# Performance work log

Measured on AMD Instinct MI355X. Metric: run time of the kernel, lower is better.

The kernel has to match this reference:

```python
import jax, jax.numpy as jnp
import numpy as np
import math

D = 1024
B, S = 4, 2048


def setup_inputs() -> dict:
    key = jax.random.key(0)
    ks = jax.random.split(key, 16)
    sc = 0.02
    def lin(k, dout, din):
        kw, kb = jax.random.split(k)
        return (sc * jax.random.normal(kw, (dout, din), jnp.float32),
                sc * jax.random.normal(kb, (dout,), jnp.float32))
    Wq, bq = lin(ks[0], D, D)
    Wk, bk = lin(ks[1], D, D)
    Wv, bv = lin(ks[2], D, D)
    Wmu, bmu = lin(ks[3], D, D)
    Wlv, blv = lin(ks[4], D, D)
    Wg, bg = lin(ks[5], 1, D)
    gamma = jnp.ones((D,), jnp.float32)
    beta = jnp.zeros((D,), jnp.float32)
    x = jax.random.normal(ks[6], (B, S, D), jnp.float32)
    eps = jax.random.normal(ks[7], (B, S, D), jnp.float32)
    return dict(x=x, eps=eps, Wq=Wq, bq=bq, Wk=Wk, bk=bk, Wv=Wv, bv=bv,
                Wmu=Wmu, bmu=bmu, Wlv=Wlv, blv=blv, Wg=Wg, bg=bg,
                gamma=gamma, beta=beta)


def _layernorm(x, gamma, beta, eps=1e-5):
    mu = jnp.mean(x, axis=-1, keepdims=True)
    var = jnp.mean(jnp.square(x - mu), axis=-1, keepdims=True)
    return (x - mu) * jax.lax.rsqrt(var + eps) * gamma + beta


def reference(x, eps, Wq, bq, Wk, bk, Wv, bv, Wmu, bmu, Wlv, blv, Wg, bg, gamma, beta):
    d = x.shape[-1]
    Q = jnp.einsum('bsd,ed->bse', x, Wq) + bq
    K = jnp.einsum('bsd,ed->bse', x, Wk) + bk
    V = jnp.einsum('bsd,ed->bse', x, Wv) + bv
    scores = jnp.einsum('bqd,bkd->bqk', Q, K) / (math.sqrt(d) * 1.5)
    attn = jax.nn.softmax(scores, axis=-1)
    h = jnp.einsum('bqk,bkd->bqd', attn, V)
    mu = jnp.einsum('bsd,ed->bse', h, Wmu) + bmu
    logvar = jnp.einsum('bsd,ed->bse', h, Wlv) + blv
    std = jnp.exp(0.5 * logvar)
    z = jax.nn.relu(mu + eps * std)
    p_gate = jax.nn.sigmoid(jnp.einsum('bd,ed->be', h.mean(axis=1), Wg) + bg)
    out = _layernorm(x + z, gamma, beta)
    return out, mu, logvar, p_gate.squeeze(-1)
```

## Files before the change

### kernel.cpp

```cpp
#include <hip/hip_runtime.h>

typedef unsigned short u16;
typedef __attribute__((ext_vector_type(8))) short bf16x8;
typedef __attribute__((ext_vector_type(4))) float f32x4;

__device__ inline float bf2f(u16 h) {
    union { unsigned u; float f; } v; v.u = ((unsigned)h) << 16; return v.f;
}
__device__ inline u16 f2bf(float f) {
    union { float f; unsigned u; } v; v.f = f;
    unsigned r = v.u + 0x7fffu + ((v.u >> 16) & 1u);
    return (u16)(r >> 16);
}

__device__ inline void gl_lds16(const u16* g, u16* l) {
    __builtin_amdgcn_global_load_lds(
        (const __attribute__((address_space(1))) void*)g,
        (__attribute__((address_space(3))) void*)l, 16, 0, 0);
}

__global__ __launch_bounds__(256) void cvt_bf16_k(
    const float* __restrict__ s0, u16* __restrict__ d0, long long n0,
    const float* __restrict__ s1, u16* __restrict__ d1, long long n1,
    const float* __restrict__ s2, u16* __restrict__ d2, long long n2,
    const float* __restrict__ s3, u16* __restrict__ d3, long long n3)
{
    int y = blockIdx.y;
    const float* s = (y == 0) ? s0 : (y == 1) ? s1 : (y == 2) ? s2 : s3;
    u16* d         = (y == 0) ? d0 : (y == 1) ? d1 : (y == 2) ? d2 : d3;
    long long n    = (y == 0) ? n0 : (y == 1) ? n1 : (y == 2) ? n2 : n3;
    for (long long i = (long long)blockIdx.x * 256 + threadIdx.x; i < n;
         i += (long long)gridDim.x * 256) {
        float4 v = ((const float4*)s)[i];
        union { u16 h[4]; unsigned long long u; } p;
        p.h[0] = f2bf(v.x); p.h[1] = f2bf(v.y);
        p.h[2] = f2bf(v.z); p.h[3] = f2bf(v.w);
        ((unsigned long long*)d)[i] = p.u;
    }
}

#define BM 128
#define BN 128
#define BK 32

template <int COUTF32, int BIASROW>
__global__ __launch_bounds__(256, 2) void gemm_bt(
    const u16* __restrict__ A, const u16* __restrict__ Bt,
    const float* __restrict__ bias, void* __restrict__ Cv,
    int M, int N, int K, float scale,
    long long sAb, long long sBb, long long sCb)
{
    __shared__ u16 As[BM * BK];
    __shared__ u16 Bs[BN * BK];

    int b = blockIdx.z;
    int bm0 = blockIdx.x * BM;
    int bn0 = blockIdx.y * BN;
    int tid = threadIdx.x;
    int w = tid >> 6, l = tid & 63;
    int wm = (w >> 1) * 64, wn = (w & 1) * 64;
    int lane15 = l & 15, quad = l >> 4;
    int lr = l >> 2;
    int lc = (l & 3) * 8;

    f32x4 acc[4][4];
#pragma unroll
    for (int i = 0; i < 4; i++)
#pragma unroll
        for (int j = 0; j < 4; j++) acc[i][j] = (f32x4)(0.0f);

    const u16* Ag = A  + (long long)b * sAb + (long long)(bm0 + w * 32 + lr) * K + lc;
    const u16* Bg = Bt + (long long)b * sBb + (long long)(bn0 + w * 32 + lr) * K + lc;

    for (int k0 = 0; k0 < K; k0 += BK) {
        gl_lds16(Ag + k0,            &As[(w * 32) * BK]);
        gl_lds16(Ag + 16LL * K + k0, &As[(w * 32 + 16) * BK]);
        gl_lds16(Bg + k0,            &Bs[(w * 32) * BK]);
        gl_lds16(Bg + 16LL * K + k0, &Bs[(w * 32 + 16) * BK]);
        __syncthreads();

        bf16x8 af[4], bfr[4];
#pragma unroll
        for (int i = 0; i < 4; i++) {
            af[i]  = *(const bf16x8*)&As[(wm + i * 16 + lane15) * BK + quad * 8];
            bfr[i] = *(const bf16x8*)&Bs[(wn + i * 16 + lane15) * BK + quad * 8];
        }
#pragma unroll
        for (int i = 0; i < 4; i++)
#pragma unroll
            for (int j = 0; j < 4; j++)
                acc[i][j] = __builtin_amdgcn_mfma_f32_16x16x32_bf16(
                    af[i], bfr[j], acc[i][j], 0, 0, 0);
        __syncthreads();
    }

    float rowb[4][4];
    if (BIASROW) {
#pragma unroll
        for (int i = 0; i < 4; i++)
#pragma unroll
            for (int r = 0; r < 4; r++)
                rowb[i][r] = bias[bm0 + wm + i * 16 + quad * 4 + r];
    }
    u16*   C16 = (u16*)Cv   + (long long)b * sCb;
    float* C32 = (float*)Cv + (long long)b * sCb;
#pragma unroll
    for (int j = 0; j < 4; j++) {
        int col = bn0 + wn + j * 16 + lane15;
        float bvc = (!BIASROW && bias) ? bias[col] : 0.0f;
#pragma unroll
        for (int i = 0; i < 4; i++) {
            int row0 = bm0 + wm + i * 16 + quad * 4;
#pragma unroll
            for (int r = 0; r < 4; r++) {
                float bv = BIASROW ? rowb[i][r] : bvc;
                float v = acc[i][j][r] * scale + bv;
                if (COUTF32) C32[(long long)(row0 + r) * N + col] = v;
                else         C16[(long long)(row0 + r) * N + col] = f2bf(v);
            }
        }
    }
}

__global__ __launch_bounds__(256) void softmax_k(u16* __restrict__ Sc)
{
    long long row = blockIdx.x;
    u16* s = Sc + row * 2048;
    int t = threadIdx.x;

    uint4 raw = *(const uint4*)(s + t * 8);
    const u16* rp = (const u16*)&raw;
    float v[8];
    float mx = -3.4e38f;
#pragma unroll
    for (int j = 0; j < 8; j++) { v[j] = bf2f(rp[j]); mx = fmaxf(mx, v[j]); }
#pragma unroll
    for (int o = 32; o > 0; o >>= 1) mx = fmaxf(mx, __shfl_xor(mx, o));
    __shared__ float redm[4];
    if ((t & 63) == 0) redm[t >> 6] = mx;
    __syncthreads();
    mx = fmaxf(fmaxf(redm[0], redm[1]), fmaxf(redm[2], redm[3]));

    float sum = 0.0f;
#pragma unroll
    for (int j = 0; j < 8; j++) { v[j] = __expf(v[j] - mx); sum += v[j]; }
#pragma unroll
    for (int o = 32; o > 0; o >>= 1) sum += __shfl_xor(sum, o);
    __shared__ float reds[4];
    if ((t & 63) == 0) reds[t >> 6] = sum;
    __syncthreads();
    sum = reds[0] + reds[1] + reds[2] + reds[3];

    float inv = 1.0f / sum;
    u16 o8[8];
#pragma unroll
    for (int j = 0; j < 8; j++) o8[j] = f2bf(v[j] * inv);
    *(uint4*)(s + t * 8) = *(const uint4*)o8;
}

__global__ __launch_bounds__(256) void gate_partial(const u16* __restrict__ h,
                                                    const float* __restrict__ Wg,
                                                    float* __restrict__ part)
{
    int b = blockIdx.x, c = blockIdx.y;
    int t = threadIdx.x;
    int tx = t & 127;
    int ty = t >> 7;
    int d0 = tx * 8;
    const u16* hb = h + (long long)b * 2048 * 1024 + (long long)c * 16 * 1024;

    float wg[8];
#pragma unroll
    for (int j = 0; j < 8; j++) wg[j] = Wg[d0 + j];

    float acc = 0.0f;
    for (int s = ty; s < 16; s += 2) {
        bf16x8 hv = *(const bf16x8*)&hb[(long long)s * 1024 + d0];
        const u16* hp = (const u16*)&hv;
#pragma unroll
        for (int j = 0; j < 8; j++) acc += bf2f(hp[j]) * wg[j];
    }
#pragma unroll
    for (int o = 32; o > 0; o >>= 1) acc += __shfl_xor(acc, o);
    __shared__ float red[4];
    if ((t & 63) == 0) red[t >> 6] = acc;
    __syncthreads();
    if (t == 0) part[b * 128 + c] = red[0] + red[1] + red[2] + red[3];
}

__global__ void gate_final(const float* __restrict__ part,
                           const float* __restrict__ bg, float* __restrict__ outp)
{
    int t = threadIdx.x;
    if (t < 4) {
        float s = 0.0f;
        for (int c = 0; c < 128; c++) s += part[t * 128 + c];
        float v = s * (1.0f / 2048.0f) + bg[0];
        outp[t] = 1.0f / (1.0f + __expf(-v));
    }
}

__global__ __launch_bounds__(256) void epilogue_k(
    const float* __restrict__ x, const float* __restrict__ ep,
    const float* __restrict__ mu, const float* __restrict__ lv,
    const float* __restrict__ gamma, const float* __restrict__ beta,
    float* __restrict__ out)
{
    long long base = (long long)blockIdx.x * 1024;
    int t = threadIdx.x;
    float y[4];
    float sum = 0.0f, sq = 0.0f;
#pragma unroll
    for (int j = 0; j < 4; j++) {
        int i = j * 256 + t;
        float xv = x[base + i];
        float ev = ep[base + i];
        float m  = mu[base + i];
        float sd = __expf(0.5f * lv[base + i]);
        float z  = fmaxf(m + ev * sd, 0.0f);
        float yy = xv + z;
        y[j] = yy; sum += yy; sq += yy * yy;
    }
#pragma unroll
    for (int o = 32; o > 0; o >>= 1) { sum += __shfl_xor(sum, o); sq += __shfl_xor(sq, o); }
    __shared__ float rs[4], rq[4];
    if ((t & 63) == 0) { rs[t >> 6] = sum; rq[t >> 6] = sq; }
    __syncthreads();
    sum = rs[0] + rs[1] + rs[2] + rs[3];
    sq  = rq[0] + rq[1] + rq[2] + rq[3];
    float mean = sum * (1.0f / 1024.0f);
    float var  = fmaxf(sq * (1.0f / 1024.0f) - mean * mean, 0.0f);
    float rstd = rsqrtf(var + 1e-5f);
#pragma unroll
    for (int j = 0; j < 4; j++) {
        int i = j * 256 + t;
        out[base + i] = (y[j] - mean) * rstd * gamma[i] + beta[i];
    }
}

extern "C" void kernel_launch(void* const* d_in, const int* in_sizes, int n_in,
                              void* d_out, int out_size, void* d_ws, size_t ws_size,
                              hipStream_t stream)
{
    const float* x     = (const float*)d_in[0];
    const float* ep    = (const float*)d_in[1];
    const float* Wq    = (const float*)d_in[2];
    const float* bq    = (const float*)d_in[3];
    const float* Wk    = (const float*)d_in[4];
    const float* bk    = (const float*)d_in[5];
    const float* Wv    = (const float*)d_in[6];
    const float* bv    = (const float*)d_in[7];
    const float* Wmu   = (const float*)d_in[8];
    const float* bmu   = (const float*)d_in[9];
    const float* Wlv   = (const float*)d_in[10];
    const float* blv   = (const float*)d_in[11];
    const float* Wg    = (const float*)d_in[12];
    const float* bg    = (const float*)d_in[13];
    const float* gamma = (const float*)d_in[14];
    const float* beta  = (const float*)d_in[15];
    float* out = (float*)d_out;

    const int M = 8192;
    const int D = 1024;
    const int S = 2048;

    float* mu_out = out + 8388608LL;
    float* lv_out = out + 16777216LL;
    float* pg_out = out + 25165824LL;

    u16* xb   = (u16*)out;
    u16* Wqb  = (u16*)out + 8388608LL;
    u16* Wkb  = (u16*)out + 9437184LL;
    u16* Wvb  = (u16*)out + 10485760LL;
    u16* Sc   = (u16*)out;
    u16* Q    = (u16*)mu_out;
    u16* Kb   = (u16*)mu_out + 8388608LL;
    u16* Vt   = (u16*)lv_out + 8388608LL;
    u16* h    = (u16*)d_ws;
    float* part = (float*)out;
    u16* Wmub = (u16*)out + 2097152LL;
    u16* Wlvb = (u16*)out + 3145728LL;

    dim3 blk(256);

    cvt_bf16_k<<<dim3(2048, 4), blk, 0, stream>>>(
        x,  xb,  2097152LL,
        Wq, Wqb, 262144LL,
        Wk, Wkb, 262144LL,
        Wv, Wvb, 262144LL);

    gemm_bt<0, 0><<<dim3(64, 8, 1), blk, 0, stream>>>(xb, Wqb, bq, Q,  M, D, D, 1.0f, 0, 0, 0);
    gemm_bt<0, 0><<<dim3(64, 8, 1), blk, 0, stream>>>(xb, Wkb, bk, Kb, M, D, D, 1.0f, 0, 0, 0);

    gemm_bt<0, 1><<<dim3(8, 16, 4), blk, 0, stream>>>(Wvb, xb, bv, Vt, D, S, D,
        1.0f, 0, (long long)S * D, (long long)D * S);

    gemm_bt<0, 0><<<dim3(16, 16, 4), blk, 0, stream>>>(Q, Kb, nullptr, Sc, S, S, D,
        1.0f / 48.0f, (long long)S * D, (long long)S * D, (long long)S * S);

    softmax_k<<<dim3(8192), blk, 0, stream>>>(Sc);

    gemm_bt<0, 0><<<dim3(16, 8, 4), blk, 0, stream>>>(Sc, Vt, nullptr, h, S, D, S,
        1.0f, (long long)S * S, (long long)D * S, (long long)S * D);

    cvt_bf16_k<<<dim3(512, 2), blk, 0, stream>>>(
        Wmu, Wmub, 262144LL,
        Wlv, Wlvb, 262144LL,
        nullptr, nullptr, 0LL,
        nullptr, nullptr, 0LL);

    gemm_bt<1, 0><<<dim3(64, 8, 1), blk, 0, stream>>>(h, Wmub, bmu, (void*)mu_out, M, D, D, 1.0f, 0, 0, 0);
    gemm_bt<1, 0><<<dim3(64, 8, 1), blk, 0, stream>>>(h, Wlvb, blv, (void*)lv_out, M, D, D, 1.0f, 0, 0, 0);

    gate_partial<<<dim3(4, 128), blk, 0, stream>>>(h, Wg, part);
    gate_final<<<dim3(1), dim3(64), 0, stream>>>(part, bg, pg_out);

    epilogue_k<<<dim3(8192), blk, 0, stream>>>(x, ep, mu_out, lv_out, gamma, beta, out);
}
```

Measured before the change: 457.7 us.

## Replace GEMM with 256x256 double-buffered 8-wave pipelined kernel and fuse projections

```diff
diff --git a/kernel.cpp b/kernel.cpp
--- a/kernel.cpp
+++ b/kernel.cpp
@@ -18,6 +18,13 @@
         (const __attribute__((address_space(1))) void*)g,
         (__attribute__((address_space(3))) void*)l, 16, 0, 0);
 }
+
+__device__ __forceinline__ void wgbar() {
+    asm volatile("" ::: "memory");
+    __builtin_amdgcn_s_barrier();
+    asm volatile("" ::: "memory");
+}
+#define VMW(n) asm volatile("s_waitcnt vmcnt(" #n ")" ::: "memory")
 
 __global__ __launch_bounds__(256) void cvt_bf16_k(
     const float* __restrict__ s0, u16* __restrict__ d0, long long n0,
@@ -39,84 +46,143 @@
     }
 }
 
-#define BM 128
-#define BN 128
-#define BK 32
-
-template <int COUTF32, int BIASROW>
-__global__ __launch_bounds__(256, 2) void gemm_bt(
+#define STA(T, H)                                                             \
+    { const u16* g_ = Ag + (long long)((H) * 128 + w * 8 + srow) * K          \
+                      + (T) * 64 + scol;                                      \
+      u16* l_ = (u16*)&As[(T) & 1][H][w * 512];                               \
+      gl_lds16(g_, l_);                                                       \
+      gl_lds16(g_ + (long long)64 * K, l_ + 4096); }
+
+#define STB(T, H)                                                             \
+    { const u16* g_ = Bg + (long long)(bn0 + (H) * 128 + w * 8 + srow) * ldb  \
+                      + (T) * 64 + scol;                                      \
+      u16* l_ = (u16*)&Bs[(T) & 1][H][w * 512];                               \
+      gl_lds16(g_, l_);                                                       \
+      gl_lds16(g_ + (long long)64 * ldb, l_ + 4096); }
+
+#define G8_PHASE(T, MQ, NQ, STAGES, WAITS)                                    \
+    {                                                                         \
+        bf16x8 av[4][2], bvv[2][2];                                           \
+        _Pragma("unroll")                                                     \
+        for (int ii = 0; ii < 4; ii++) {                                      \
+            int row = (MQ) * 64 + ii * 16 + lane15;                           \
+            _Pragma("unroll")                                                 \
+            for (int ks = 0; ks < 2; ks++)                                    \
+                av[ii][ks] = *(const bf16x8*)&As[(T) & 1][wm2]                \
+                    [(row * 64 + ks * 32 + quad * 8) ^ xr];                   \
+        }                                                                     \
+        _Pragma("unroll")                                                     \
+        for (int jj = 0; jj < 2; jj++) {                                      \
+            int row = (wn2 & 1) * 64 + (NQ) * 32 + jj * 16 + lane15;          \
+            _Pragma("unroll")                                                 \
+            for (int ks = 0; ks < 2; ks++)                                    \
+                bvv[jj][ks] = *(const bf16x8*)&Bs[(T) & 1][wn2 >> 1]          \
+                    [(row * 64 + ks * 32 + quad * 8) ^ xr];                   \
+        }                                                                     \
+        STAGES;                                                               \
+        WAITS;                                                                \
+        wgbar();                                                              \
+        __builtin_amdgcn_s_setprio(1);                                        \
+        _Pragma("unroll")                                                     \
+        for (int ii = 0; ii < 4; ii++)                                        \
+            _Pragma("unroll")                                                 \
+            for (int jj = 0; jj < 2; jj++) {                                  \
+                acc[(MQ)*4+ii][(NQ)*2+jj] =                                   \
+                    __builtin_amdgcn_mfma_f32_16x16x32_bf16(                  \
+                        av[ii][0], bvv[jj][0], acc[(MQ)*4+ii][(NQ)*2+jj],     \
+                        0, 0, 0);                                             \
+                acc[(MQ)*4+ii][(NQ)*2+jj] =                                   \
+                    __builtin_amdgcn_mfma_f32_16x16x32_bf16(                  \
+                        av[ii][1], bvv[jj][1], acc[(MQ)*4+ii][(NQ)*2+jj],     \
+                        0, 0, 0);                                             \
+            }                                                                 \
+        __builtin_amdgcn_s_setprio(0);                                        \
+        wgbar();                                                              \
+    }
+
+template <int COUTF32, int BIASROW, int NSPLIT>
+__global__ __launch_bounds__(512, 2) void gemm8(
     const u16* __restrict__ A, const u16* __restrict__ Bt,
-    const float* __restrict__ bias, void* __restrict__ Cv,
-    int M, int N, int K, float scale,
-    long long sAb, long long sBb, long long sCb)
-{
-    __shared__ u16 As[BM * BK];
-    __shared__ u16 Bs[BN * BK];
-
-    int b = blockIdx.z;
-    int bm0 = blockIdx.x * BM;
-    int bn0 = blockIdx.y * BN;
+    const float* __restrict__ bias0, const float* __restrict__ bias1,
+    const float* __restrict__ bias2,
+    void* __restrict__ C0, void* __restrict__ C1, void* __restrict__ C2,
+    int M, int N, int K, int ldb, float scale,
+    long long sAb, long long sBb, long long sCb, long long bofs_stride)
+{
+    __shared__ u16 As[2][2][8192];
+    __shared__ u16 Bs[2][2][8192];
+
+    int b   = blockIdx.z;
+    int bm0 = blockIdx.x * 256;
+    int bn0 = blockIdx.y * 256;
     int tid = threadIdx.x;
     int w = tid >> 6, l = tid & 63;
-    int wm = (w >> 1) * 64, wn = (w & 1) * 64;
+    int wm2 = w >> 2;
+    int wn2 = w & 3;
     int lane15 = l & 15, quad = l >> 4;
-    int lr = l >> 2;
-    int lc = (l & 3) * 8;
-
-    f32x4 acc[4][4];
-#pragma unroll
-    for (int i = 0; i < 4; i++)
+    int xr = (l & 7) << 3;
+
+    int srow = l >> 3;
+    int scol = ((l & 7) ^ (srow & 7)) * 8;
+
+    const u16* Ag = A  + (long long)b * sAb + (long long)bm0 * K;
+    const u16* Bg = Bt + (long long)b * sBb + (long long)(bm0 >> 11) * bofs_stride;
+
+    f32x4 acc[8][4];
+#pragma unroll
+    for (int i = 0; i < 8; i++)
 #pragma unroll
         for (int j = 0; j < 4; j++) acc[i][j] = (f32x4)(0.0f);
 
-    const u16* Ag = A  + (long long)b * sAb + (long long)(bm0 + w * 32 + lr) * K + lc;
-    const u16* Bg = Bt + (long long)b * sBb + (long long)(bn0 + w * 32 + lr) * K + lc;
-
-    for (int k0 = 0; k0 < K; k0 += BK) {
-        gl_lds16(Ag + k0,            &As[(w * 32) * BK]);
-        gl_lds16(Ag + 16LL * K + k0, &As[(w * 32 + 16) * BK]);
-        gl_lds16(Bg + k0,            &Bs[(w * 32) * BK]);
-        gl_lds16(Bg + 16LL * K + k0, &Bs[(w * 32 + 16) * BK]);
-        __syncthreads();
-
-        bf16x8 af[4], bfr[4];
-#pragma unroll
-        for (int i = 0; i < 4; i++) {
-            af[i]  = *(const bf16x8*)&As[(wm + i * 16 + lane15) * BK + quad * 8];
-            bfr[i] = *(const bf16x8*)&Bs[(wn + i * 16 + lane15) * BK + quad * 8];
-        }
-#pragma unroll
-        for (int i = 0; i < 4; i++)
-#pragma unroll
-            for (int j = 0; j < 4; j++)
-                acc[i][j] = __builtin_amdgcn_mfma_f32_16x16x32_bf16(
-                    af[i], bfr[j], acc[i][j], 0, 0, 0);
-        __syncthreads();
-    }
-
-    float rowb[4][4];
+    int NT  = K >> 6;
+    int NT2 = K >> 7;
+
+    STA(0, 0); STA(0, 1); STB(0, 0); STB(0, 1); STA(1, 1);
+    VMW(2);
+    wgbar();
+
+    for (int j = 0; j < NT2; ++j) {
+        int t0 = 2 * j, t1 = 2 * j + 1;
+        bool nl = (j < NT2 - 1);
+        G8_PHASE(t0, 0, 0, STA(t1, 0), );
+        G8_PHASE(t0, 0, 1, STB(t1, 0), );
+        G8_PHASE(t0, 1, 1, STB(t1, 1), );
+        G8_PHASE(t0, 1, 0, if (nl) STA(t0 + 2, 0),
+                 if (nl) { VMW(2); } else { VMW(0); });
+        G8_PHASE(t1, 1, 0, if (nl) STA(t0 + 2, 1), );
+        G8_PHASE(t1, 1, 1, if (nl) STB(t0 + 2, 0), );
+        G8_PHASE(t1, 0, 1, if (nl) STB(t0 + 2, 1), );
+        G8_PHASE(t1, 0, 0, if (nl) STA(t0 + 3, 1),
+                 if (nl) { VMW(2); } else { VMW(0); });
+    }
+
+    float rowb_[8][4];
     if (BIASROW) {
 #pragma unroll
-        for (int i = 0; i < 4; i++)
+        for (int i = 0; i < 8; i++)
 #pragma unroll
             for (int r = 0; r < 4; r++)
-                rowb[i][r] = bias[bm0 + wm + i * 16 + quad * 4 + r];
-    }
-    u16*   C16 = (u16*)Cv   + (long long)b * sCb;
-    float* C32 = (float*)Cv + (long long)b * sCb;
-#pragma unroll
-    for (int j = 0; j < 4; j++) {
-        int col = bn0 + wn + j * 16 + lane15;
-        float bvc = (!BIASROW && bias) ? bias[col] : 0.0f;
-#pragma unroll
-        for (int i = 0; i < 4; i++) {
-            int row0 = bm0 + wm + i * 16 + quad * 4;
+                rowb_[i][r] = bias0[bm0 + wm2 * 128 + i * 16 + quad * 4 + r];
+    }
+#pragma unroll
+    for (int jj = 0; jj < 4; jj++) {
+        int col = bn0 + wn2 * 64 + jj * 16 + lane15;
+        int seg, cl, cstride;
+        if (NSPLIT == 1) { seg = 0; cl = col; cstride = N; }
+        else             { seg = col >> 10; cl = col & 1023; cstride = 1024; }
+        const float* bp = (seg == 0) ? bias0 : (seg == 1 ? bias1 : bias2);
+        void* cb = (seg == 0) ? C0 : (seg == 1 ? C1 : C2);
+        u16*   c16 = (u16*)cb   + (long long)b * sCb;
+        float* c32 = (float*)cb + (long long)b * sCb;
+        float bvc = (!BIASROW && bp) ? bp[cl] : 0.0f;
+#pragma unroll
+        for (int i = 0; i < 8; i++) {
+            int row0 = bm0 + wm2 * 128 + i * 16 + quad * 4;
 #pragma unroll
             for (int r = 0; r < 4; r++) {
-                float bv = BIASROW ? rowb[i][r] : bvc;
-                float v = acc[i][j][r] * scale + bv;
-                if (COUTF32) C32[(long long)(row0 + r) * N + col] = v;
-                else         C16[(long long)(row0 + r) * N + col] = f2bf(v);
+                float v = acc[i][jj][r] * scale + (BIASROW ? rowb_[i][r] : bvc);
+                if (COUTF32) c32[(long long)(row0 + r) * cstride + cl] = v;
+                else         c16[(long long)(row0 + r) * cstride + cl] = f2bf(v);
             }
         }
     }
@@ -275,13 +341,13 @@
     u16* Sc   = (u16*)out;
     u16* Q    = (u16*)mu_out;
     u16* Kb   = (u16*)mu_out + 8388608LL;
-    u16* Vt   = (u16*)lv_out + 8388608LL;
+    u16* Vt   = (u16*)lv_out;
     u16* h    = (u16*)d_ws;
     float* part = (float*)out;
     u16* Wmub = (u16*)out + 2097152LL;
     u16* Wlvb = (u16*)out + 3145728LL;
 
-    dim3 blk(256);
+    dim3 blk(256), blk8(512);
 
     cvt_bf16_k<<<dim3(2048, 4), blk, 0, stream>>>(
         x,  xb,  2097152LL,
@@ -289,19 +355,24 @@
         Wk, Wkb, 262144LL,
         Wv, Wvb, 262144LL);
 
-    gemm_bt<0, 0><<<dim3(64, 8, 1), blk, 0, stream>>>(xb, Wqb, bq, Q,  M, D, D, 1.0f, 0, 0, 0);
-    gemm_bt<0, 0><<<dim3(64, 8, 1), blk, 0, stream>>>(xb, Wkb, bk, Kb, M, D, D, 1.0f, 0, 0, 0);
-
-    gemm_bt<0, 1><<<dim3(8, 16, 4), blk, 0, stream>>>(Wvb, xb, bv, Vt, D, S, D,
-        1.0f, 0, (long long)S * D, (long long)D * S);
-
-    gemm_bt<0, 0><<<dim3(16, 16, 4), blk, 0, stream>>>(Q, Kb, nullptr, Sc, S, S, D,
-        1.0f / 48.0f, (long long)S * D, (long long)S * D, (long long)S * S);
+    gemm8<0, 0, 2><<<dim3(32, 8, 1), blk8, 0, stream>>>(
+        xb, Wqb, bq, bk, nullptr, Q, Kb, nullptr,
+        M, 2048, D, D, 1.0f, 0, 0, 0, 0);
+
+    gemm8<0, 1, 1><<<dim3(4, 32, 1), blk8, 0, stream>>>(
+        Wvb, xb, bv, nullptr, nullptr, Vt, nullptr, nullptr,
+        D, 8192, D, D, 1.0f, 0, 0, 0, 0);
+
+    gemm8<0, 0, 1><<<dim3(8, 8, 4), blk8, 0, stream>>>(
+        Q, Kb, nullptr, nullptr, nullptr, Sc, nullptr, nullptr,
+        S, S, D, D, 1.0f / 48.0f,
+        (long long)S * D, (long long)S * D, (long long)S * S, 0);
 
     softmax_k<<<dim3(8192), blk, 0, stream>>>(Sc);
 
-    gemm_bt<0, 0><<<dim3(16, 8, 4), blk, 0, stream>>>(Sc, Vt, nullptr, h, S, D, S,
-        1.0f, (long long)S * S, (long long)D * S, (long long)S * D);
+    gemm8<0, 0, 1><<<dim3(32, 4, 1), blk8, 0, stream>>>(
+        Sc, Vt, nullptr, nullptr, nullptr, h, nullptr, nullptr,
+        M, D, S, 8192, 1.0f, 0, 0, 0, 2048);
 
     cvt_bf16_k<<<dim3(512, 2), blk, 0, stream>>>(
         Wmu, Wmub, 262144LL,
@@ -309,8 +380,9 @@
         nullptr, nullptr, 0LL,
         nullptr, nullptr, 0LL);
 
-    gemm_bt<1, 0><<<dim3(64, 8, 1), blk, 0, stream>>>(h, Wmub, bmu, (void*)mu_out, M, D, D, 1.0f, 0, 0, 0);
-    gemm_bt<1, 0><<<dim3(64, 8, 1), blk, 0, stream>>>(h, Wlvb, blv, (void*)lv_out, M, D, D, 1.0f, 0, 0, 0);
+    gemm8<1, 0, 2><<<dim3(32, 8, 1), blk8, 0, stream>>>(
+        h, Wmub, bmu, blv, nullptr, (void*)mu_out, (void*)lv_out, nullptr,
+        M, 2048, D, D, 1.0f, 0, 0, 0, 0);
 
     gate_partial<<<dim3(4, 128), blk, 0, stream>>>(h, Wg, part);
     gate_final<<<dim3(1), dim3(64), 0, stream>>>(part, bg, pg_out);
```

Result: slower. 483.3 us (+5.6%).

## Replace GEMM with 512-thread triple-buffered swizzled kernel and fuse paired projections

Applied to the files above, without the earlier changes.

```diff
diff --git a/kernel.cpp b/kernel.cpp
--- a/kernel.cpp
+++ b/kernel.cpp
@@ -18,6 +18,13 @@
         (const __attribute__((address_space(1))) void*)g,
         (__attribute__((address_space(3))) void*)l, 16, 0, 0);
 }
+
+__device__ __forceinline__ void wgbar() {
+    asm volatile("" ::: "memory");
+    __builtin_amdgcn_s_barrier();
+    asm volatile("" ::: "memory");
+}
+#define VMW(n) asm volatile("s_waitcnt vmcnt(" #n ")" ::: "memory")
 
 __global__ __launch_bounds__(256) void cvt_bf16_k(
     const float* __restrict__ s0, u16* __restrict__ d0, long long n0,
@@ -39,29 +46,71 @@
     }
 }
 
-#define BM 128
-#define BN 128
-#define BK 32
-
-template <int COUTF32, int BIASROW>
-__global__ __launch_bounds__(256, 2) void gemm_bt(
+#define STA(T, SL2, S)                                                        \
+    { const u16* g_ = Ag + (long long)((S) * 64 + w * 8 + srow) * K           \
+                      + (long long)(T) * 64 + scol;                           \
+      gl_lds16(g_, &As[SL2][(S) * 4096 + w * 512]); }
+
+#define STB(T, SL2, S)                                                        \
+    { const u16* g_ = Bg + (long long)(bn0 + (S) * 64 + w * 8 + srow) * ldb   \
+                      + (long long)(T) * 64 + scol;                           \
+      gl_lds16(g_, &Bs[SL2][(S) * 4096 + w * 512]); }
+
+#define G8_READS(SL, KS)                                                      \
+    bf16x8 av[4], bvv[4];                                                     \
+    _Pragma("unroll")                                                         \
+    for (int ii = 0; ii < 4; ii++)                                            \
+        av[ii] = *(const bf16x8*)&As[SL][                                     \
+            ((wm * 64 + ii * 16 + lane15) * 64 + (KS) * 32 + quad * 8) ^ xr]; \
+    _Pragma("unroll")                                                         \
+    for (int jj = 0; jj < 4; jj++)                                            \
+        bvv[jj] = *(const bf16x8*)&Bs[SL][                                    \
+            ((wn * 64 + jj * 16 + lane15) * 64 + (KS) * 32 + quad * 8) ^ xr];
+
+#define G8_MMA                                                                \
+    __builtin_amdgcn_s_setprio(1);                                            \
+    _Pragma("unroll")                                                         \
+    for (int ii = 0; ii < 4; ii++)                                            \
+        _Pragma("unroll")                                                     \
+        for (int jj = 0; jj < 4; jj++)                                        \
+            acc[ii][jj] = __builtin_amdgcn_mfma_f32_16x16x32_bf16(            \
+                av[ii], bvv[jj], acc[ii][jj], 0, 0, 0);                       \
+    __builtin_amdgcn_s_setprio(0);
+
+template <int COUTF32, int BIASROW, int NSPLIT>
+__global__ __launch_bounds__(512, 2) void gemm8(
     const u16* __restrict__ A, const u16* __restrict__ Bt,
-    const float* __restrict__ bias, void* __restrict__ Cv,
-    int M, int N, int K, float scale,
-    long long sAb, long long sBb, long long sCb)
-{
-    __shared__ u16 As[BM * BK];
-    __shared__ u16 Bs[BN * BK];
-
-    int b = blockIdx.z;
-    int bm0 = blockIdx.x * BM;
-    int bn0 = blockIdx.y * BN;
+    const float* __restrict__ bias0, const float* __restrict__ bias1,
+    void* __restrict__ C0, void* __restrict__ C1,
+    int M, int N, int K, int ldb, float scale,
+    long long sAb, long long sBb, long long sCb, long long bofs_stride)
+{
+    __shared__ u16 As[3][8192];
+    __shared__ u16 Bs[3][16384];
+
+    int gx = gridDim.x, gy = gridDim.y;
+    int n = gx * gy * gridDim.z;
+    int flat = (blockIdx.z * gy + blockIdx.y) * gx + blockIdx.x;
+    int L = (flat & 7) * (n >> 3) + (flat >> 3);
+    int bz = L / (gx * gy);
+    int rr = L - bz * gx * gy;
+    int by = rr / gx, bx = rr - (rr / gx) * gx;
+
+    int bm0 = bx * 128;
+    int bn0 = by * 256;
+    int b   = bz;
     int tid = threadIdx.x;
     int w = tid >> 6, l = tid & 63;
-    int wm = (w >> 1) * 64, wn = (w & 1) * 64;
+    int wm = w >> 2;
+    int wn = w & 3;
     int lane15 = l & 15, quad = l >> 4;
-    int lr = l >> 2;
-    int lc = (l & 3) * 8;
+    int xr = (l & 7) << 3;
+
+    int srow = l >> 3;
+    int scol = ((l & 7) ^ srow) * 8;
+
+    const u16* Ag = A  + (long long)b * sAb + (long long)bm0 * K;
+    const u16* Bg = Bt + (long long)b * sBb + (long long)(bm0 >> 11) * bofs_stride;
 
     f32x4 acc[4][4];
 #pragma unroll
@@ -69,54 +118,69 @@
 #pragma unroll
         for (int j = 0; j < 4; j++) acc[i][j] = (f32x4)(0.0f);
 
-    const u16* Ag = A  + (long long)b * sAb + (long long)(bm0 + w * 32 + lr) * K + lc;
-    const u16* Bg = Bt + (long long)b * sBb + (long long)(bn0 + w * 32 + lr) * K + lc;
-
-    for (int k0 = 0; k0 < K; k0 += BK) {
-        gl_lds16(Ag + k0,            &As[(w * 32) * BK]);
-        gl_lds16(Ag + 16LL * K + k0, &As[(w * 32 + 16) * BK]);
-        gl_lds16(Bg + k0,            &Bs[(w * 32) * BK]);
-        gl_lds16(Bg + 16LL * K + k0, &Bs[(w * 32 + 16) * BK]);
-        __syncthreads();
-
-        bf16x8 af[4], bfr[4];
+    int NT = K >> 6;
+
+    STA(0, 0, 0); STA(0, 0, 1);
+    STB(0, 0, 0); STB(0, 0, 1); STB(0, 0, 2); STB(0, 0, 3);
+    STA(1, 1, 0); STA(1, 1, 1);
+    STB(1, 1, 0); STB(1, 1, 1); STB(1, 1, 2); STB(1, 1, 3);
+    VMW(6);
+    wgbar();
+
+    int sl = 0, sl2 = 2;
+    for (int t = 0; t < NT; ++t) {
+        bool pf = (t + 2 < NT);
+        int t2 = t + 2;
+        {
+            G8_READS(sl, 0);
+            if (pf) { STA(t2, sl2, 0); STA(t2, sl2, 1); STB(t2, sl2, 0); }
+            wgbar();
+            G8_MMA;
+            wgbar();
+        }
+        {
+            G8_READS(sl, 1);
+            if (pf) {
+                STB(t2, sl2, 1); STB(t2, sl2, 2); STB(t2, sl2, 3);
+                VMW(6);
+            } else {
+                VMW(0);
+            }
+            wgbar();
+            G8_MMA;
+            wgbar();
+        }
+        sl  = (sl  == 2) ? 0 : sl + 1;
+        sl2 = (sl2 == 2) ? 0 : sl2 + 1;
+    }
+
+    float rowb_[4][4];
+    if (BIASROW) {
+#pragma unroll
+        for (int i = 0; i < 4; i++)
+#pragma unroll
+            for (int r = 0; r < 4; r++)
+                rowb_[i][r] = bias0[bm0 + wm * 64 + i * 16 + quad * 4 + r];
+    }
+#pragma unroll
+    for (int jj = 0; jj < 4; jj++) {
+        int col = bn0 + wn * 64 + jj * 16 + lane15;
+        int seg, cl, cstride;
+        if (NSPLIT == 1) { seg = 0; cl = col; cstride = N; }
+        else             { seg = col >> 10; cl = col & 1023; cstride = 1024; }
+        const float* bp = (seg == 0) ? bias0 : bias1;
+        void* cb = (seg == 0) ? C0 : C1;
+        u16*   c16 = (u16*)cb   + (long long)b * sCb;
+        float* c32 = (float*)cb + (long long)b * sCb;
+        float bvc = (!BIASROW && bp) ? bp[cl] : 0.0f;
 #pragma unroll
         for (int i = 0; i < 4; i++) {
-            af[i]  = *(const bf16x8*)&As[(wm + i * 16 + lane15) * BK + quad * 8];
-            bfr[i] = *(const bf16x8*)&Bs[(wn + i * 16 + lane15) * BK + quad * 8];
-        }
-#pragma unroll
-        for (int i = 0; i < 4; i++)
-#pragma unroll
-            for (int j = 0; j < 4; j++)
-                acc[i][j] = __builtin_amdgcn_mfma_f32_16x16x32_bf16(
-                    af[i], bfr[j], acc[i][j], 0, 0, 0);
-        __syncthreads();
-    }
-
-    float rowb[4][4];
-    if (BIASROW) {
-#pragma unroll
-        for (int i = 0; i < 4; i++)
-#pragma unroll
-            for (int r = 0; r < 4; r++)
-                rowb[i][r] = bias[bm0 + wm + i * 16 + quad * 4 + r];
-    }
-    u16*   C16 = (u16*)Cv   + (long long)b * sCb;
-    float* C32 = (float*)Cv + (long long)b * sCb;
-#pragma unroll
-    for (int j = 0; j < 4; j++) {
-        int col = bn0 + wn + j * 16 + lane15;
-        float bvc = (!BIASROW && bias) ? bias[col] : 0.0f;
-#pragma unroll
-        for (int i = 0; i < 4; i++) {
-            int row0 = bm0 + wm + i * 16 + quad * 4;
+            int row0 = bm0 + wm * 64 + i * 16 + quad * 4;
 #pragma unroll
             for (int r = 0; r < 4; r++) {
-                float bv = BIASROW ? rowb[i][r] : bvc;
-                float v = acc[i][j][r] * scale + bv;
-                if (COUTF32) C32[(long long)(row0 + r) * N + col] = v;
-                else         C16[(long long)(row0 + r) * N + col] = f2bf(v);
+                float v = acc[i][jj][r] * scale + (BIASROW ? rowb_[i][r] : bvc);
+                if (COUTF32) c32[(long long)(row0 + r) * cstride + cl] = v;
+                else         c16[(long long)(row0 + r) * cstride + cl] = f2bf(v);
             }
         }
     }
@@ -275,13 +339,13 @@
     u16* Sc   = (u16*)out;
     u16* Q    = (u16*)mu_out;
     u16* Kb   = (u16*)mu_out + 8388608LL;
-    u16* Vt   = (u16*)lv_out + 8388608LL;
+    u16* Vt   = (u16*)lv_out;
     u16* h    = (u16*)d_ws;
     float* part = (float*)out;
     u16* Wmub = (u16*)out + 2097152LL;
     u16* Wlvb = (u16*)out + 3145728LL;
 
-    dim3 blk(256);
+    dim3 blk(256), blk8(512);
 
     cvt_bf16_k<<<dim3(2048, 4), blk, 0, stream>>>(
         x,  xb,  2097152LL,
@@ -289,19 +353,24 @@
         Wk, Wkb, 262144LL,
         Wv, Wvb, 262144LL);
 
-    gemm_bt<0, 0><<<dim3(64, 8, 1), blk, 0, stream>>>(xb, Wqb, bq, Q,  M, D, D, 1.0f, 0, 0, 0);
-    gemm_bt<0, 0><<<dim3(64, 8, 1), blk, 0, stream>>>(xb, Wkb, bk, Kb, M, D, D, 1.0f, 0, 0, 0);
-
-    gemm_bt<0, 1><<<dim3(8, 16, 4), blk, 0, stream>>>(Wvb, xb, bv, Vt, D, S, D,
-        1.0f, 0, (long long)S * D, (long long)D * S);
-
-    gemm_bt<0, 0><<<dim3(16, 16, 4), blk, 0, stream>>>(Q, Kb, nullptr, Sc, S, S, D,
-        1.0f / 48.0f, (long long)S * D, (long long)S * D, (long long)S * S);
+    gemm8<0, 0, 2><<<dim3(64, 8, 1), blk8, 0, stream>>>(
+        xb, Wqb, bq, bk, Q, Kb,
+        M, 2048, D, D, 1.0f, 0, 0, 0, 0);
+
+    gemm8<0, 1, 1><<<dim3(8, 32, 1), blk8, 0, stream>>>(
+        Wvb, xb, bv, nullptr, Vt, nullptr,
+        D, 8192, D, D, 1.0f, 0, 0, 0, 0);
+
+    gemm8<0, 0, 1><<<dim3(16, 8, 4), blk8, 0, stream>>>(
+        Q, Kb, nullptr, nullptr, Sc, nullptr,
+        S, S, D, D, 1.0f / 48.0f,
+        (long long)S * D, (long long)S * D, (long long)S * S, 0);
 
     softmax_k<<<dim3(8192), blk, 0, stream>>>(Sc);
 
-    gemm_bt<0, 0><<<dim3(16, 8, 4), blk, 0, stream>>>(Sc, Vt, nullptr, h, S, D, S,
-        1.0f, (long long)S * S, (long long)D * S, (long long)S * D);
+    gemm8<0, 0, 1><<<dim3(64, 4, 1), blk8, 0, stream>>>(
+        Sc, Vt, nullptr, nullptr, h, nullptr,
+        M, D, S, 8192, 1.0f, 0, 0, 0, 2048);
 
     cvt_bf16_k<<<dim3(512, 2), blk, 0, stream>>>(
         Wmu, Wmub, 262144LL,
@@ -309,8 +378,9 @@
         nullptr, nullptr, 0LL,
         nullptr, nullptr, 0LL);
 
-    gemm_bt<1, 0><<<dim3(64, 8, 1), blk, 0, stream>>>(h, Wmub, bmu, (void*)mu_out, M, D, D, 1.0f, 0, 0, 0);
-    gemm_bt<1, 0><<<dim3(64, 8, 1), blk, 0, stream>>>(h, Wlvb, blv, (void*)lv_out, M, D, D, 1.0f, 0, 0, 0);
+    gemm8<1, 0, 2><<<dim3(64, 8, 1), blk8, 0, stream>>>(
+        h, Wmub, bmu, blv, (void*)mu_out, (void*)lv_out,
+        M, 2048, D, D, 1.0f, 0, 0, 0, 0);
 
     gate_partial<<<dim3(4, 128), blk, 0, stream>>>(h, Wg, part);
     gate_final<<<dim3(1), dim3(64), 0, stream>>>(part, bg, pg_out);
```

New measurement: 423.9 us. 7.4% less time.
